# Optimization experiments

Hardware: AMD Instinct MI355X
Metric: run time of the kernel (lower is better)

## Reference

```python
import jax, jax.numpy as jnp
import numpy as np

B=64; HW=14; E=2048; L=30; V=10000; EMB=512; AML=768; ADL=500
D=512+ADL   # decoder_dim + article_downlen = 1012
A=512+ADL   # attention_dim + article_downlen = 1012

def setup_inputs() -> dict:
    key = jax.random.key(0)
    ks = jax.random.split(key, 20)
    s = 0.02
    lin = lambda k, i, o: (jax.random.normal(k, (i, o), jnp.float32) * s)
    inp = {}
    inp['encoder_out'] = jax.random.normal(ks[0], (B, HW, HW, E), jnp.float32)
    inp['encoded_captions'] = jax.random.randint(ks[1], (B, L), 0, V)
    cl = jax.random.randint(ks[2], (B, 1), 2, L + 1)
    inp['caption_lengths'] = cl.at[0, 0].set(L)  # ensure max decode length == L-1
    inp['encoded_articles'] = jax.random.normal(ks[3], (B, 1, AML), jnp.float32)
    inp['article_lengths'] = jax.random.randint(ks[4], (B, 1), 1, AML)
    inp['blank_context'] = 0
    inp['E_emb'] = jax.random.uniform(ks[5], (V, EMB), jnp.float32, -0.1, 0.1)
    inp['W_par'] = lin(ks[6], AML, ADL); inp['b_par'] = jnp.zeros(ADL, jnp.float32)
    inp['W_enc'] = lin(ks[7], E, A);     inp['b_enc'] = jnp.zeros(A, jnp.float32)
    inp['W_dec'] = lin(ks[8], D, A);     inp['b_dec'] = jnp.zeros(A, jnp.float32)
    inp['W_full'] = lin(ks[9], A, 1);    inp['b_full'] = jnp.zeros(1, jnp.float32)
    inp['W_h'] = lin(ks[10], E + ADL, D); inp['b_h'] = jnp.zeros(D, jnp.float32)
    inp['W_c'] = lin(ks[11], E + ADL, D); inp['b_c'] = jnp.zeros(D, jnp.float32)
    inp['W_fb'] = lin(ks[12], D, E);      inp['b_fb'] = jnp.zeros(E, jnp.float32)
    inp['W_ih'] = lin(ks[13], EMB + E, 4 * D); inp['b_ih'] = jnp.zeros(4 * D, jnp.float32)
    inp['W_hh'] = lin(ks[14], D, 4 * D);       inp['b_hh'] = jnp.zeros(4 * D, jnp.float32)
    inp['W_fc'] = jax.random.uniform(ks[15], (D, V), jnp.float32, -0.1, 0.1)
    inp['b_fc'] = jnp.zeros(V, jnp.float32)
    return inp

def reference(encoder_out, encoded_captions, caption_lengths, encoded_articles,
              article_lengths, blank_context, E_emb, W_par, b_par, W_enc, b_enc,
              W_dec, b_dec, W_full, b_full, W_h, b_h, W_c, b_c, W_fb, b_fb,
              W_ih, b_ih, W_hh, b_hh, W_fc, b_fc):
    Bv = encoder_out.shape[0]
    enc = encoder_out.reshape(Bv, -1, encoder_out.shape[-1])  # (B, P, E)
    lens = caption_lengths[:, 0]
    sort_ind = jnp.argsort(-lens)
    lens = lens[sort_ind]
    enc = enc[sort_ind]
    caps = encoded_captions[sort_ind]
    arts = encoded_articles[sort_ind]
    emb = E_emb[caps]                                   # (B, L, EMB)
    context = (arts @ W_par + b_par)[:, 0, :]           # ParagraphEncoder -> (B, ADL)
    dec_in = jnp.concatenate([enc.mean(axis=1), context], axis=1)
    h0 = dec_in @ W_h + b_h
    c0 = dec_in @ W_c + b_c
    dlens = lens - 1
    att1 = enc @ W_enc + b_enc                          # loop-invariant, (B, P, A)
    T = emb.shape[1] - 1

    def step(carry, t):
        h, c = carry
        active = (dlens > t)[:, None]                   # prefix mask (sorted desc)
        att2 = h @ W_dec + b_dec
        scores = (jax.nn.relu(att1 + att2[:, None, :]) @ W_full)[..., 0] + b_full[0]
        alpha = jax.nn.softmax(scores, axis=1)          # (B, P)
        awe = jnp.einsum('bp,bpe->be', alpha, enc)
        awe = jax.nn.sigmoid(h @ W_fb + b_fb) * awe     # gated attention encoding
        x = jnp.concatenate([emb[:, t, :], awe], axis=1)
        gates = x @ W_ih + b_ih + h @ W_hh + b_hh       # torch LSTMCell, gate order i,f,g,o
        i, f, g, o = jnp.split(gates, 4, axis=1)
        c_new = jax.nn.sigmoid(f) * c + jax.nn.sigmoid(i) * jnp.tanh(g)
        h_new = jax.nn.sigmoid(o) * jnp.tanh(c_new)
        preds = jnp.where(active, h_new @ W_fc + b_fc, 0.0)
        alpha_m = jnp.where(active, alpha, 0.0)
        h = jnp.where(active, h_new, h)
        c = jnp.where(active, c_new, c)
        return (h, c), (preds, alpha_m)

    _, (preds, alphas) = jax.lax.scan(step, (h0, c0), jnp.arange(T))
    predictions = jnp.transpose(preds, (1, 0, 2))       # (B, T, V)
    alphas = jnp.transpose(alphas, (1, 0, 2))           # (B, T, P)
    return (predictions, caps, dlens, alphas, sort_ind)
```

## Files before the change

kernel.cpp:

```cpp
#include <hip/hip_runtime.h>
#include <math.h>

#define B_   64
#define P_   196
#define E_   2048
#define L_   30
#define T_   29
#define V_   10000
#define EMB_ 512
#define AML_ 768
#define ADL_ 500
#define D_   1012
#define A_   1012
#define G4_  4048
#define XK_  2560

typedef unsigned short u16;
typedef __attribute__((ext_vector_type(8))) short bf16x8;
typedef __attribute__((ext_vector_type(4))) float f32x4;

__device__ __forceinline__ float sigf(float x) { return 1.f / (1.f + __expf(-x)); }
__device__ __forceinline__ float tanhf_fast(float x) { return 1.f - 2.f / (__expf(2.f * x) + 1.f); }
__device__ __forceinline__ u16 f2bf(float f) {
    unsigned u = __float_as_uint(f);
    return (u16)((u + 0x7FFFu + ((u >> 16) & 1u)) >> 16);
}
__device__ __forceinline__ float bf2f(u16 v) { return __uint_as_float(((unsigned)v) << 16); }

__global__ void k_setup(const int* __restrict__ clen, const int* __restrict__ caps,
                        float* __restrict__ out_caps, float* __restrict__ out_dlens,
                        float* __restrict__ out_sind,
                        int* __restrict__ sort_ind, int* __restrict__ dlens_i,
                        int* __restrict__ nact, int* __restrict__ caps_s)
{
    __shared__ int lens[B_];
    int t = threadIdx.x;
    if (t < B_) lens[t] = clen[t];
    __syncthreads();
    if (t < B_) {
        int my = lens[t];
        int rank = 0;
        for (int j = 0; j < B_; ++j) {
            int lj = lens[j];
            if (lj > my || (lj == my && j < t)) rank++;
        }
        sort_ind[rank] = t;
    }
    __syncthreads();
    if (t < B_) {
        int orig = sort_ind[t];
        int dl = lens[orig] - 1;
        dlens_i[t] = dl;
        out_dlens[t] = (float)dl;
        out_sind[t] = (float)orig;
        for (int j = 0; j < L_; ++j) {
            int cv = caps[orig * L_ + j];
            caps_s[t * L_ + j] = cv;
            out_caps[t * L_ + j] = (float)cv;
        }
    }
    __syncthreads();
    if (t < T_) {
        int cnt = 0;
        for (int j = 0; j < B_; ++j) cnt += (dlens_i[j] > t) ? 1 : 0;
        nact[t] = cnt;
    }
}

__global__ void k_zero(float4* __restrict__ p, long n4)
{
    long i = (long)blockIdx.x * 256 + threadIdx.x;
    if (i < n4) p[i] = make_float4(0.f, 0.f, 0.f, 0.f);
}

__global__ void k_cvt_enc(const float* __restrict__ enc, const int* __restrict__ sort_ind,
                          u16* __restrict__ A_bf)
{
    int row = blockIdx.y;
    int b = row / 196, p = row - b * 196;
    int e4 = (blockIdx.x * 256 + threadIdx.x) * 4;
    const float* src = enc + ((long)sort_ind[b] * 196 + p) * E_ + e4;
    float4 v = *(const float4*)src;
    unsigned lo = (unsigned)f2bf(v.x) | ((unsigned)f2bf(v.y) << 16);
    unsigned hi = (unsigned)f2bf(v.z) | ((unsigned)f2bf(v.w) << 16);
    uint2 pk; pk.x = lo; pk.y = hi;
    *(uint2*)(A_bf + (long)row * E_ + e4) = pk;
}

__global__ void k_transpose(const float* __restrict__ src, u16* __restrict__ dst,
                            int K, int N, int Kp, int Np)
{
    __shared__ float tile[32][33];
    int n0 = blockIdx.x * 32, k0 = blockIdx.y * 32;
    int tx = threadIdx.x, ty = threadIdx.y;
    for (int r = ty; r < 32; r += 8) {
        int k = k0 + r, n = n0 + tx;
        tile[r][tx] = (k < K && n < N) ? src[(long)k * N + n] : 0.f;
    }
    __syncthreads();
    for (int r = ty; r < 32; r += 8) {
        int n = n0 + r, k = k0 + tx;
        if (n < Np && k < Kp) dst[(long)n * Kp + k] = f2bf(tile[tx][r]);
    }
}

__global__ void k_encmean(const float* __restrict__ enc, const int* __restrict__ sort_ind,
                          u16* __restrict__ dec_in)
{
    int b = blockIdx.y;
    int e = blockIdx.x * 256 + threadIdx.x;
    int orig = sort_ind[b];
    const float* src = enc + (long)orig * P_ * E_ + e;
    float s = 0.f;
    for (int p = 0; p < P_; ++p) s += src[(long)p * E_];
    dec_in[(long)b * XK_ + e] = f2bf(s * (1.f / 196.f));
}

__global__ void k_ctx(const float* __restrict__ arts, const float* __restrict__ W_par,
                      const float* __restrict__ b_par, const int* __restrict__ sort_ind,
                      u16* __restrict__ dec_in)
{
    int b = blockIdx.y;
    int k = blockIdx.x * 256 + threadIdx.x;
    if (k >= 512) return;
    float s = 0.f;
    if (k < ADL_) {
        int orig = sort_ind[b];
        const float* ar = arts + (long)orig * AML_;
        s = b_par[k];
        for (int m = 0; m < AML_; ++m) s = fmaf(ar[m], W_par[m * ADL_ + k], s);
    }
    dec_in[(long)b * XK_ + E_ + k] = f2bf(s);
}

__global__ void k_emb_all(const float* __restrict__ E_emb, const int* __restrict__ caps_s,
                          u16* __restrict__ emb_all)
{
    int t = blockIdx.x;
    int b = blockIdx.y;
    int tok = caps_s[b * L_ + t];
    for (int k = threadIdx.x; k < EMB_; k += 256)
        emb_all[((long)t * B_ + b) * EMB_ + k] = f2bf(E_emb[(long)tok * EMB_ + k]);
}

__global__ void __launch_bounds__(256) k_att1_mfma(
    const u16* __restrict__ A, const u16* __restrict__ W,
    const float* __restrict__ bias, u16* __restrict__ Yb)
{
    __shared__ u16 As[2][64][40];
    int w = threadIdx.x >> 6, lane = threadIdx.x & 63;
    int lr = lane & 15, lk = (lane >> 4) * 8;
    int n0 = blockIdx.x * 256 + w * 64;
    int r0 = blockIdx.y * 64;
    int arow = threadIdx.x >> 2;
    int akseg = (threadIdx.x & 3) * 8;
    const u16* ag = A + (long)(r0 + arow) * E_ + akseg;

    f32x4 acc[4][4];
#pragma unroll
    for (int i = 0; i < 4; ++i)
#pragma unroll
        for (int j = 0; j < 4; ++j) acc[i][j] = (f32x4){0.f, 0.f, 0.f, 0.f};
    const u16* wp = W + (long)(n0 + lr) * E_ + lk;

    *(uint2*)&As[0][arow][akseg] = *(const uint2*)(ag);
    __syncthreads();

    for (int k = 0; k < E_; k += 32) {
        int buf = (k >> 5) & 1;
        bool more = (k + 32) < E_;
        uint2 pre;
        if (more) pre = *(const uint2*)(ag + k + 32);
        bf16x8 bf[4], af[4];
#pragma unroll
        for (int nt = 0; nt < 4; ++nt) bf[nt] = *(const bf16x8*)(wp + (long)nt * 16 * E_ + k);
#pragma unroll
        for (int mt = 0; mt < 4; ++mt) af[mt] = *(const bf16x8*)&As[buf][mt * 16 + lr][lk];
#pragma unroll
        for (int mt = 0; mt < 4; ++mt)
#pragma unroll
            for (int nt = 0; nt < 4; ++nt)
                acc[mt][nt] = __builtin_amdgcn_mfma_f32_16x16x32_bf16(af[mt], bf[nt], acc[mt][nt], 0, 0, 0);
        if (more) *(uint2*)&As[buf ^ 1][arow][akseg] = pre;
        __syncthreads();
    }
#pragma unroll
    for (int mt = 0; mt < 4; ++mt) {
#pragma unroll
        for (int nt = 0; nt < 4; ++nt) {
            int n = n0 + nt * 16 + lr;
            float bv = (n < A_) ? bias[n] : 0.f;
#pragma unroll
            for (int j = 0; j < 4; ++j) {
                int row = r0 + mt * 16 + (lane >> 4) * 4 + j;
                u16 outv = (n < A_) ? f2bf(acc[mt][nt][j] + bv) : (u16)0;
                Yb[(long)row * 1024 + n] = outv;
            }
        }
    }
}

template <int ACT, int OUT, int PADZ>
__global__ void __launch_bounds__(256) k_skinny(
    const u16* __restrict__ A1, const u16* __restrict__ W1, int K1,
    const float* __restrict__ bias1, void* __restrict__ Yv,
    long ldY, long offY, int Nmax,
    const int* __restrict__ nact, int t)
{
    int Bact = (t >= 0) ? nact[t] : B_;
    if (Bact <= 0) return;
    int mmax = (Bact + 15) >> 4;
    int w = threadIdx.x >> 6, lane = threadIdx.x & 63;
    int lr = lane & 15, lk = (lane >> 4) * 8;
    int n0 = blockIdx.x * 64 + w * 16;
    f32x4 acc[4];
#pragma unroll
    for (int m = 0; m < 4; ++m) acc[m] = (f32x4){0.f, 0.f, 0.f, 0.f};

    int n = n0 + lr;
    int nc = n < Nmax ? n : Nmax - 1;
    const u16* a1p = A1 + (long)lr * K1 + lk;
    const u16* w1p = W1 + (long)nc * K1 + lk;
    for (int k = 0; k < K1; k += 32) {
        bf16x8 bw = *(const bf16x8*)(w1p + k);
#pragma unroll
        for (int m = 0; m < 4; ++m)
            if (m < mmax) {
                bf16x8 aw = *(const bf16x8*)(a1p + (long)m * 16 * K1 + k);
                acc[m] = __builtin_amdgcn_mfma_f32_16x16x32_bf16(aw, bw, acc[m], 0, 0, 0);
            }
    }
    float bv = (n < Nmax) ? bias1[n] : 0.f;
#pragma unroll
    for (int m = 0; m < 4; ++m) {
        if (m < mmax) {
#pragma unroll
            for (int j = 0; j < 4; ++j) {
                int b = m * 16 + (lane >> 4) * 4 + j;
                if (b < Bact) {
                    float v = acc[m][j] + bv;
                    if (ACT == 1) v = sigf(v);
                    if (n < Nmax) {
                        if (OUT == 1) ((u16*)Yv)[(long)b * ldY + offY + n] = f2bf(v);
                        else          ((float*)Yv)[(long)b * ldY + offY + n] = v;
                    } else if (PADZ) {
                        if (OUT == 1) ((u16*)Yv)[(long)b * ldY + offY + n] = 0;
                        else          ((float*)Yv)[(long)b * ldY + offY + n] = 0.f;
                    }
                }
            }
        }
    }
}

__global__ void __launch_bounds__(256) k_gemb(
    const u16* __restrict__ emb_all, const u16* __restrict__ WT_ih,
    float* __restrict__ gemb_all)
{
    int t = blockIdx.y;
    int w = threadIdx.x >> 6, lane = threadIdx.x & 63;
    int lr = lane & 15, lk = (lane >> 4) * 8;
    int n0 = blockIdx.x * 256 + w * 64;
    f32x4 acc[4][4];
#pragma unroll
    for (int i = 0; i < 4; ++i)
#pragma unroll
        for (int j = 0; j < 4; ++j) acc[i][j] = (f32x4){0.f, 0.f, 0.f, 0.f};
    const u16* ap = emb_all + ((long)t * B_ + lr) * EMB_ + lk;
    long wrow[4];
#pragma unroll
    for (int nt = 0; nt < 4; ++nt) {
        int j = n0 + nt * 16 + lr;
        int q = j >> 10, d = j & 1023;
        wrow[nt] = (long)q * D_ + (d < D_ ? d : D_ - 1);
    }
    for (int k = 0; k < EMB_; k += 32) {
        bf16x8 af[4], bf[4];
#pragma unroll
        for (int mt = 0; mt < 4; ++mt) af[mt] = *(const bf16x8*)(ap + (long)mt * 16 * EMB_ + k);
#pragma unroll
        for (int nt = 0; nt < 4; ++nt) bf[nt] = *(const bf16x8*)(WT_ih + wrow[nt] * XK_ + lk + k);
#pragma unroll
        for (int mt = 0; mt < 4; ++mt)
#pragma unroll
            for (int nt = 0; nt < 4; ++nt)
                acc[mt][nt] = __builtin_amdgcn_mfma_f32_16x16x32_bf16(af[mt], bf[nt], acc[mt][nt], 0, 0, 0);
    }
#pragma unroll
    for (int nt = 0; nt < 4; ++nt) {
        int j = n0 + nt * 16 + lr;
#pragma unroll
        for (int mt = 0; mt < 4; ++mt) {
#pragma unroll
            for (int jj = 0; jj < 4; ++jj) {
                int b = mt * 16 + (lane >> 4) * 4 + jj;
                gemb_all[((long)t * B_ + b) * 4096 + j] = acc[mt][nt][jj];
            }
        }
    }
}

__global__ void __launch_bounds__(256) k_att2fb(
    const u16* __restrict__ h_bf, const u16* __restrict__ WT_dec,
    const u16* __restrict__ WT_fb, const float* __restrict__ b_dec,
    const float* __restrict__ b_fb, float* __restrict__ att2p,
    float* __restrict__ fbp, const int* __restrict__ nact, int t)
{
    int Bact = nact[t];
    if (Bact <= 0) return;
    int mmax = (Bact + 15) >> 4;
    int kh = blockIdx.x >= 48;
    int nb = blockIdx.x - (kh ? 48 : 0);
    int isfb = nb >= 16;
    const u16* W = isfb ? WT_fb : WT_dec;
    const float* bias = isfb ? b_fb : b_dec;
    int Nmax = isfb ? E_ : A_;
    int nb2 = isfb ? nb - 16 : nb;
    long ldY = isfb ? (long)E_ : 1024L;
    float* Y = (isfb ? fbp : att2p) + (long)kh * B_ * ldY;

    int w = threadIdx.x >> 6, lane = threadIdx.x & 63;
    int lr = lane & 15, lk = (lane >> 4) * 8;
    int n = nb2 * 64 + w * 16 + lr;
    int nc = n < Nmax ? n : Nmax - 1;
    int k0 = kh * 512;
    f32x4 acc[4];
#pragma unroll
    for (int m = 0; m < 4; ++m) acc[m] = (f32x4){0.f, 0.f, 0.f, 0.f};
    const u16* ap = h_bf + (long)lr * 1024 + k0 + lk;
    const u16* wp = W + (long)nc * 1024 + k0 + lk;
    for (int k = 0; k < 512; k += 32) {
        bf16x8 bw = *(const bf16x8*)(wp + k);
#pragma unroll
        for (int m = 0; m < 4; ++m)
            if (m < mmax) {
                bf16x8 aw = *(const bf16x8*)(ap + (long)m * 16 * 1024 + k);
                acc[m] = __builtin_amdgcn_mfma_f32_16x16x32_bf16(aw, bw, acc[m], 0, 0, 0);
            }
    }
    if (n >= Nmax) return;
    float bv = (kh == 0) ? bias[n] : 0.f;
#pragma unroll
    for (int m = 0; m < 4; ++m) {
        if (m < mmax) {
#pragma unroll
            for (int j = 0; j < 4; ++j) {
                int b = m * 16 + (lane >> 4) * 4 + j;
                if (b < Bact) Y[(long)b * ldY + n] = acc[m][j] + bv;
            }
        }
    }
}

__global__ void k_scores(const u16* __restrict__ att1, const float* __restrict__ att2p,
                         const float* __restrict__ W_full, const float* __restrict__ b_full,
                         float* __restrict__ scores, const int* __restrict__ nact, int t)
{
    int b = blockIdx.y;
    if (b >= nact[t]) return;
    int wv = threadIdx.x >> 6;
    int lane = threadIdx.x & 63;
    int p = blockIdx.x * 4 + wv;
    const u16* a1 = att1 + ((long)b * P_ + p) * 1024;
    const float* a20 = att2p + (long)b * 1024;
    const float* a21 = att2p + (long)B_ * 1024 + (long)b * 1024;
    float acc = 0.f;
    for (int j2 = lane; j2 < 506; j2 += 64) {
        unsigned pk = *(const unsigned*)(a1 + 2 * j2);
        float2 p0 = *(const float2*)(a20 + 2 * j2);
        float2 p1 = *(const float2*)(a21 + 2 * j2);
        float2 wv2 = *(const float2*)(W_full + 2 * j2);
        float v0 = bf2f((u16)(pk & 0xFFFF)) + p0.x + p1.x;
        float v1 = bf2f((u16)(pk >> 16)) + p0.y + p1.y;
        v0 = v0 > 0.f ? v0 : 0.f;
        v1 = v1 > 0.f ? v1 : 0.f;
        acc = fmaf(v0, wv2.x, acc);
        acc = fmaf(v1, wv2.y, acc);
    }
    for (int m = 32; m >= 1; m >>= 1) acc += __shfl_xor(acc, m);
    if (lane == 0) scores[b * P_ + p] = acc + b_full[0];
}

__global__ void __launch_bounds__(256) k_awe_x(
    const u16* __restrict__ A_bf, const float* __restrict__ scores,
    const float* __restrict__ fbp, u16* __restrict__ awe_buf,
    float* __restrict__ alphas_out, const int* __restrict__ nact, int t)
{
    int b = blockIdx.y;
    if (b >= nact[t]) return;
    int tid = threadIdx.x;
    int w = tid >> 6, lane = tid & 63;
    __shared__ float al[P_];
    __shared__ float red[4];
    float v = (tid < P_) ? scores[b * P_ + tid] : -1e30f;
    float m = v;
    for (int s = 32; s >= 1; s >>= 1) m = fmaxf(m, __shfl_xor(m, s));
    if (lane == 0) red[w] = m;
    __syncthreads();
    m = fmaxf(fmaxf(red[0], red[1]), fmaxf(red[2], red[3]));
    float e = (tid < P_) ? __expf(v - m) : 0.f;
    float s_ = e;
    for (int s = 32; s >= 1; s >>= 1) s_ += __shfl_xor(s_, s);
    __syncthreads();
    if (lane == 0) red[w] = s_;
    __syncthreads();
    s_ = red[0] + red[1] + red[2] + red[3];
    if (tid < P_) al[tid] = e / s_;
    __syncthreads();

    if (blockIdx.x < 8) {
        int e0 = blockIdx.x * 256 + tid;
        const u16* src = A_bf + (long)b * P_ * E_ + e0;
        float s0 = 0.f, s1 = 0.f, s2 = 0.f, s3 = 0.f;
        for (int p = 0; p < P_; p += 4) {
            s0 = fmaf(al[p],     bf2f(src[(long)p * E_]), s0);
            s1 = fmaf(al[p + 1], bf2f(src[(long)(p + 1) * E_]), s1);
            s2 = fmaf(al[p + 2], bf2f(src[(long)(p + 2) * E_]), s2);
            s3 = fmaf(al[p + 3], bf2f(src[(long)(p + 3) * E_]), s3);
        }
        long fb_off = (long)b * E_ + e0;
        float g = sigf(fbp[fb_off] + fbp[131072 + fb_off]);
        awe_buf[(long)b * E_ + e0] = f2bf((s0 + s1 + s2 + s3) * g);
    } else {
        if (tid < P_) alphas_out[((long)b * T_ + t) * P_ + tid] = al[tid];
    }
}

__global__ void __launch_bounds__(256) k_gates(
    const u16* __restrict__ awe, const u16* __restrict__ h_old,
    const u16* __restrict__ WT_ih, const u16* __restrict__ WT_hh,
    float* __restrict__ gpart, const int* __restrict__ nact, int t)
{
    int Bact = nact[t];
    if (Bact <= 0) return;
    int mmax = (Bact + 15) >> 4;
    int q = threadIdx.x >> 6;
    int lane = threadIdx.x & 63;
    int lr = lane & 15, lk = (lane >> 4) * 8;
    int kh = blockIdx.y;
    int n = blockIdx.x * 16 + lr;
    int nc = n < D_ ? n : D_ - 1;
    f32x4 acc[4];
#pragma unroll
    for (int m = 0; m < 4; ++m) acc[m] = (f32x4){0.f, 0.f, 0.f, 0.f};
    const u16* wih = WT_ih + ((long)q * D_ + nc) * XK_;
    const u16* whh = WT_hh + ((long)q * D_ + nc) * 1024;

    if (kh == 0) {
        const u16* ap = awe + (long)lr * E_ + lk;
        const u16* w2 = wih + 512;
        for (int k = 0; k < 1536; k += 32) {
            bf16x8 bw = *(const bf16x8*)(w2 + k);
#pragma unroll
            for (int m = 0; m < 4; ++m)
                if (m < mmax) {
                    bf16x8 aw = *(const bf16x8*)(ap + (long)m * 16 * E_ + k);
                    acc[m] = __builtin_amdgcn_mfma_f32_16x16x32_bf16(aw, bw, acc[m], 0, 0, 0);
                }
        }
    } else {
        const u16* ap2 = awe + (long)lr * E_ + 1536 + lk;
        const u16* w2 = wih + 2048;
        for (int k = 0; k < 512; k += 32) {
            bf16x8 bw = *(const bf16x8*)(w2 + k);
#pragma unroll
            for (int m = 0; m < 4; ++m)
                if (m < mmax) {
                    bf16x8 aw = *(const bf16x8*)(ap2 + (long)m * 16 * E_ + k);
                    acc[m] = __builtin_amdgcn_mfma_f32_16x16x32_bf16(aw, bw, acc[m], 0, 0, 0);
                }
        }
        const u16* ap3 = h_old + (long)lr * 1024 + lk;
        for (int k = 0; k < 1024; k += 32) {
            bf16x8 bw = *(const bf16x8*)(whh + k);
#pragma unroll
            for (int m = 0; m < 4; ++m)
                if (m < mmax) {
                    bf16x8 aw = *(const bf16x8*)(ap3 + (long)m * 16 * 1024 + k);
                    acc[m] = __builtin_amdgcn_mfma_f32_16x16x32_bf16(aw, bw, acc[m], 0, 0, 0);
                }
        }
    }
#pragma unroll
    for (int m = 0; m < 4; ++m) {
        if (m < mmax) {
#pragma unroll
            for (int j = 0; j < 4; ++j) {
                int bb = m * 16 + (lane >> 4) * 4 + j;
                if (bb < Bact)
                    gpart[((long)kh * B_ + bb) * 4096 + q * 1024 + n] = acc[m][j];
            }
        }
    }
}

__global__ void k_lstm_red(const float* __restrict__ gpart, const float* __restrict__ gemb_t,
                           const float* __restrict__ b_ih, const float* __restrict__ b_hh,
                           float* __restrict__ cbuf, u16* __restrict__ h_new,
                           const int* __restrict__ nact, int t)
{
    int b = blockIdx.y;
    if (b >= nact[t]) return;
    int n = blockIdx.x * 256 + threadIdx.x;
    if (n >= D_) return;
    const float* g0 = gpart + (long)b * 4096;
    const float* g1 = gpart + (long)(B_ + b) * 4096;
    const float* ge = gemb_t + (long)b * 4096;
    float gi = g0[n]        + g1[n]        + ge[n]        + b_ih[n]          + b_hh[n];
    float gf = g0[1024 + n] + g1[1024 + n] + ge[1024 + n] + b_ih[D_ + n]     + b_hh[D_ + n];
    float gg = g0[2048 + n] + g1[2048 + n] + ge[2048 + n] + b_ih[2 * D_ + n] + b_hh[2 * D_ + n];
    float go = g0[3072 + n] + g1[3072 + n] + ge[3072 + n] + b_ih[3 * D_ + n] + b_hh[3 * D_ + n];
    float c = cbuf[(long)b * 1024 + n];
    float cn = sigf(gf) * c + sigf(gi) * tanhf_fast(gg);
    float hn = sigf(go) * tanhf_fast(cn);
    cbuf[(long)b * 1024 + n] = cn;
    h_new[(long)b * 1024 + n] = f2bf(hn);
}

__global__ void __launch_bounds__(256) k_fc_all(
    const u16* __restrict__ h_all, const u16* __restrict__ W,
    const float* __restrict__ bias, float* __restrict__ out_preds,
    const int* __restrict__ nact)
{
    int tslot = blockIdx.y;
    int Bact = nact[tslot];
    if (Bact <= 0) return;
    int mmax = (Bact + 15) >> 4;
    int w = threadIdx.x >> 6, lane = threadIdx.x & 63;
    int lr = lane & 15, lk = (lane >> 4) * 8;
    int n0 = blockIdx.x * 256 + w * 64;
    f32x4 acc[4][4];
#pragma unroll
    for (int i = 0; i < 4; ++i)
#pragma unroll
        for (int j = 0; j < 4; ++j) acc[i][j] = (f32x4){0.f, 0.f, 0.f, 0.f};
    const u16* ap = h_all + ((long)(tslot + 1) * B_ + lr) * 1024 + lk;
    int ncl[4];
#pragma unroll
    for (int nt = 0; nt < 4; ++nt) {
        int n = n0 + nt * 16 + lr;
        ncl[nt] = n < V_ ? n : V_ - 1;
    }
    for (int k = 0; k < 1024; k += 32) {
        bf16x8 af[4], bf[4];
#pragma unroll
        for (int mt = 0; mt < 4; ++mt)
            if (mt < mmax) af[mt] = *(const bf16x8*)(ap + (long)mt * 16 * 1024 + k);
#pragma unroll
        for (int nt = 0; nt < 4; ++nt) bf[nt] = *(const bf16x8*)(W + (long)ncl[nt] * 1024 + lk + k);
#pragma unroll
        for (int mt = 0; mt < 4; ++mt)
            if (mt < mmax)
#pragma unroll
                for (int nt = 0; nt < 4; ++nt)
                    acc[mt][nt] = __builtin_amdgcn_mfma_f32_16x16x32_bf16(af[mt], bf[nt], acc[mt][nt], 0, 0, 0);
    }
#pragma unroll
    for (int nt = 0; nt < 4; ++nt) {
        int n = n0 + nt * 16 + lr;
        if (n >= V_) continue;
        float bv = bias[n];
#pragma unroll
        for (int mt = 0; mt < 4; ++mt) {
            if (mt < mmax) {
#pragma unroll
                for (int j = 0; j < 4; ++j) {
                    int b = mt * 16 + (lane >> 4) * 4 + j;
                    if (b < Bact)
                        out_preds[(long)b * T_ * V_ + (long)tslot * V_ + n] = acc[mt][nt][j] + bv;
                }
            }
        }
    }
}

extern "C" void kernel_launch(void* const* d_in, const int* in_sizes, int n_in,
                              void* d_out, int out_size, void* d_ws, size_t ws_size,
                              hipStream_t stream)
{
    const float* enc    = (const float*)d_in[0];
    const int*   caps   = (const int*)d_in[1];
    const int*   clen   = (const int*)d_in[2];
    const float* arts   = (const float*)d_in[3];
    const float* E_emb  = (const float*)d_in[6];
    const float* W_par  = (const float*)d_in[7];
    const float* b_par  = (const float*)d_in[8];
    const float* W_enc  = (const float*)d_in[9];
    const float* b_enc  = (const float*)d_in[10];
    const float* W_dec  = (const float*)d_in[11];
    const float* b_dec  = (const float*)d_in[12];
    const float* W_full = (const float*)d_in[13];
    const float* b_full = (const float*)d_in[14];
    const float* W_h    = (const float*)d_in[15];
    const float* b_h    = (const float*)d_in[16];
    const float* W_c    = (const float*)d_in[17];
    const float* b_c    = (const float*)d_in[18];
    const float* W_fb   = (const float*)d_in[19];
    const float* b_fb   = (const float*)d_in[20];
    const float* W_ih   = (const float*)d_in[21];
    const float* b_ih   = (const float*)d_in[22];
    const float* W_hh   = (const float*)d_in[23];
    const float* b_hh   = (const float*)d_in[24];
    const float* W_fc   = (const float*)d_in[25];
    const float* b_fc   = (const float*)d_in[26];

    float* out = (float*)d_out;
    float* out_preds  = out;
    float* out_caps   = out + (long)B_ * T_ * V_;
    float* out_dlens  = out_caps + B_ * L_;
    float* out_alphas = out_dlens + B_;
    float* out_sind   = out_alphas + (long)B_ * T_ * P_;

    float* ws = (float*)d_ws;
    long o = 0;
    auto alloc = [&](long n) { long r = o; o += (n + 63) & ~63L; return r; };
    long o_ints   = alloc(2176);
    long o_decin  = alloc((long)B_ * XK_ / 2);
    long o_hall   = alloc((long)(T_ + 1) * B_ * 1024 / 2);
    long o_emball = alloc((long)T_ * B_ * EMB_ / 2);
    long o_awe    = alloc((long)B_ * E_ / 2);
    long o_c      = alloc((long)B_ * 1024);
    long o_att2p  = alloc((long)2 * B_ * 1024);
    long o_fbp    = alloc((long)2 * B_ * E_);
    long o_gpart  = alloc((long)2 * B_ * 4096);
    long o_gemb   = alloc((long)T_ * B_ * 4096);
    long o_scores = alloc((long)B_ * P_);
    long o_Abf    = alloc((long)12544 * E_ / 2);
    long o_att1   = alloc((long)12544 * 1024 / 2);
    long o_wtenc  = alloc((long)1024 * 2048 / 2);
    long o_wtdec  = alloc((long)1024 * 1024 / 2);
    long o_wtfb   = alloc((long)2048 * 1024 / 2);
    long o_wtih   = alloc((long)4096 * 2560 / 2);
    long o_wthh   = alloc((long)4096 * 1024 / 2);
    long o_wtfc   = alloc((long)10048 * 1024 / 2);

    int* sort_ind = (int*)(ws + o_ints);
    int* dlens_i  = sort_ind + 64;
    int* nact     = dlens_i + 64;
    int* caps_s   = nact + 32;
    u16*   dec_in  = (u16*)(ws + o_decin);
    u16*   h_all   = (u16*)(ws + o_hall);
    u16*   emb_all = (u16*)(ws + o_emball);
    u16*   awe_buf = (u16*)(ws + o_awe);
    float* cbuf   = ws + o_c;
    float* att2p  = ws + o_att2p;
    float* fbp    = ws + o_fbp;
    float* gpart  = ws + o_gpart;
    float* gemb_all = ws + o_gemb;
    float* scores = ws + o_scores;
    u16*   A_bf   = (u16*)(ws + o_Abf);
    u16*   att1   = (u16*)(ws + o_att1);
    u16*   WT_enc = (u16*)(ws + o_wtenc);
    u16*   WT_dec = (u16*)(ws + o_wtdec);
    u16*   WT_fb  = (u16*)(ws + o_wtfb);
    u16*   WT_ih  = (u16*)(ws + o_wtih);
    u16*   WT_hh  = (u16*)(ws + o_wthh);
    u16*   WT_fc  = (u16*)(ws + o_wtfc);
    u16*   WT_h   = att1;
    u16*   WT_c   = att1 + (long)1024 * XK_;

    long n4 = ((long)B_ * T_ * V_ + B_ * L_ + B_ + (long)B_ * T_ * P_ + B_) / 4;
    k_zero<<<dim3((unsigned)((n4 + 255) / 256)), 256, 0, stream>>>((float4*)d_out, n4);
    k_setup<<<1, 64, 0, stream>>>(clen, caps, out_caps, out_dlens, out_sind,
                                  sort_ind, dlens_i, nact, caps_s);

    k_encmean<<<dim3(8, 64), 256, 0, stream>>>(enc, sort_ind, dec_in);
    k_ctx<<<dim3(2, 64), 256, 0, stream>>>(arts, W_par, b_par, sort_ind, dec_in);
    k_emb_all<<<dim3(T_, 64), 256, 0, stream>>>(E_emb, caps_s, emb_all);

    dim3 tb(32, 8);
    k_transpose<<<dim3(1024/32, 2560/32), tb, 0, stream>>>(W_h, WT_h, 2548, 1012, 2560, 1024);
    k_transpose<<<dim3(1024/32, 2560/32), tb, 0, stream>>>(W_c, WT_c, 2548, 1012, 2560, 1024);
    k_skinny<0,1,1><<<dim3(16), 256, 0, stream>>>(dec_in, WT_h, XK_, b_h, h_all, 1024L, 0L, D_,
                                                  nact, -1);
    k_skinny<0,0,1><<<dim3(16), 256, 0, stream>>>(dec_in, WT_c, XK_, b_c, cbuf, 1024L, 0L, D_,
                                                  nact, -1);

    k_transpose<<<dim3(1024/32, 2048/32), tb, 0, stream>>>(W_enc, WT_enc, 2048, 1012, 2048, 1024);
    k_transpose<<<dim3(1024/32, 1024/32), tb, 0, stream>>>(W_dec, WT_dec, 1012, 1012, 1024, 1024);
    k_transpose<<<dim3(2048/32, 1024/32), tb, 0, stream>>>(W_fb, WT_fb, 1012, 2048, 1024, 2048);
    k_transpose<<<dim3(4096/32, 2560/32), tb, 0, stream>>>(W_ih, WT_ih, 2560, 4048, 2560, 4096);
    k_transpose<<<dim3(4096/32, 1024/32), tb, 0, stream>>>(W_hh, WT_hh, 1012, 4048, 1024, 4096);
    k_transpose<<<dim3(10048/32, 1024/32), tb, 0, stream>>>(W_fc, WT_fc, 1012, 10000, 1024, 10048);

    k_cvt_enc<<<dim3(2, 12544), 256, 0, stream>>>(enc, sort_ind, A_bf);
    k_att1_mfma<<<dim3(4, 196), 256, 0, stream>>>(A_bf, WT_enc, b_enc, att1);
    k_gemb<<<dim3(16, T_), 256, 0, stream>>>(emb_all, WT_ih, gemb_all);

    for (int t = 0; t < T_; ++t) {
        const u16* h_old = h_all + (long)t * B_ * 1024;
        u16* h_new = h_all + (long)(t + 1) * B_ * 1024;
        const float* gemb_t = gemb_all + (long)t * B_ * 4096;
        k_att2fb<<<dim3(96), 256, 0, stream>>>(h_old, WT_dec, WT_fb, b_dec, b_fb,
                                               att2p, fbp, nact, t);
        k_scores<<<dim3(49, 64), 256, 0, stream>>>(att1, att2p, W_full, b_full, scores, nact, t);
        k_awe_x<<<dim3(9, 64), 256, 0, stream>>>(A_bf, scores, fbp, awe_buf,
                                                 out_alphas, nact, t);
        k_gates<<<dim3(64, 2), 256, 0, stream>>>(awe_buf, h_old, WT_ih, WT_hh, gpart, nact, t);
        k_lstm_red<<<dim3(4, 64), 256, 0, stream>>>(gpart, gemb_t, b_ih, b_hh, cbuf, h_new,
                                                    nact, t);
    }
    k_fc_all<<<dim3(40, T_), 256, 0, stream>>>(h_all, WT_fc, b_fc, out_preds, nact);
}
```

Baseline: 2.847 ms.

## Move h·W_hh into att2/fb kernel and fuse LSTM reduction into gates

The recurrent h@W_hh product is now computed in the kernel that already reads h for att2 and the gate signal, as 128 extra blocks that write partial sums to a new ghp buffer. This leaves the gates kernel with a balanced 1024+1024 split over the awe part of W_ih. The separate LSTM elementwise kernel is removed: the last of the two k-split blocks per column tile, found with an atomic counter, sums all partials and applies the cell update. The goal is one fewer launch per step and better balanced work on the critical path, at the cost of a threadfence/atomic handshake and an extra partial buffer. The att1 GEMM tile load is also widened from uint2 to uint4, so each thread now fills its full 8-element slice of the shared tile.

Measured after the change: 2.979 ms. 4.6% more time.

```diff
diff --git a/kernel.cpp b/kernel.cpp
--- a/kernel.cpp
+++ b/kernel.cpp
@@ -31,11 +31,13 @@
                         float* __restrict__ out_caps, float* __restrict__ out_dlens,
                         float* __restrict__ out_sind,
                         int* __restrict__ sort_ind, int* __restrict__ dlens_i,
-                        int* __restrict__ nact, int* __restrict__ caps_s)
+                        int* __restrict__ nact, int* __restrict__ caps_s,
+                        int* __restrict__ gcnt)
 {
     __shared__ int lens[B_];
     int t = threadIdx.x;
     if (t < B_) lens[t] = clen[t];
+    if (t < 64) gcnt[t] = 0;
     __syncthreads();
     if (t < B_) {
         int my = lens[t];
@@ -163,14 +165,14 @@
         for (int j = 0; j < 4; ++j) acc[i][j] = (f32x4){0.f, 0.f, 0.f, 0.f};
     const u16* wp = W + (long)(n0 + lr) * E_ + lk;
 
-    *(uint2*)&As[0][arow][akseg] = *(const uint2*)(ag);
+    *(uint4*)&As[0][arow][akseg] = *(const uint4*)(ag);
     __syncthreads();
 
     for (int k = 0; k < E_; k += 32) {
         int buf = (k >> 5) & 1;
         bool more = (k + 32) < E_;
-        uint2 pre;
-        if (more) pre = *(const uint2*)(ag + k + 32);
+        uint4 pre;
+        if (more) pre = *(const uint4*)(ag + k + 32);
         bf16x8 bf[4], af[4];
 #pragma unroll
         for (int nt = 0; nt < 4; ++nt) bf[nt] = *(const bf16x8*)(wp + (long)nt * 16 * E_ + k);
@@ -181,7 +183,7 @@
 #pragma unroll
             for (int nt = 0; nt < 4; ++nt)
                 acc[mt][nt] = __builtin_amdgcn_mfma_f32_16x16x32_bf16(af[mt], bf[nt], acc[mt][nt], 0, 0, 0);
-        if (more) *(uint2*)&As[buf ^ 1][arow][akseg] = pre;
+        if (more) *(uint4*)&As[buf ^ 1][arow][akseg] = pre;
         __syncthreads();
     }
 #pragma unroll
@@ -300,53 +302,89 @@
     }
 }
 
-__global__ void __launch_bounds__(256) k_att2fb(
+__global__ void __launch_bounds__(256) k_hg(
     const u16* __restrict__ h_bf, const u16* __restrict__ WT_dec,
-    const u16* __restrict__ WT_fb, const float* __restrict__ b_dec,
-    const float* __restrict__ b_fb, float* __restrict__ att2p,
-    float* __restrict__ fbp, const int* __restrict__ nact, int t)
+    const u16* __restrict__ WT_fb, const u16* __restrict__ WT_hh,
+    const float* __restrict__ b_dec, const float* __restrict__ b_fb,
+    float* __restrict__ att2p, float* __restrict__ fbp, float* __restrict__ ghp,
+    const int* __restrict__ nact, int t)
 {
     int Bact = nact[t];
     if (Bact <= 0) return;
     int mmax = (Bact + 15) >> 4;
-    int kh = blockIdx.x >= 48;
-    int nb = blockIdx.x - (kh ? 48 : 0);
-    int isfb = nb >= 16;
-    const u16* W = isfb ? WT_fb : WT_dec;
-    const float* bias = isfb ? b_fb : b_dec;
-    int Nmax = isfb ? E_ : A_;
-    int nb2 = isfb ? nb - 16 : nb;
-    long ldY = isfb ? (long)E_ : 1024L;
-    float* Y = (isfb ? fbp : att2p) + (long)kh * B_ * ldY;
-
     int w = threadIdx.x >> 6, lane = threadIdx.x & 63;
     int lr = lane & 15, lk = (lane >> 4) * 8;
-    int n = nb2 * 64 + w * 16 + lr;
-    int nc = n < Nmax ? n : Nmax - 1;
-    int k0 = kh * 512;
-    f32x4 acc[4];
-#pragma unroll
-    for (int m = 0; m < 4; ++m) acc[m] = (f32x4){0.f, 0.f, 0.f, 0.f};
-    const u16* ap = h_bf + (long)lr * 1024 + k0 + lk;
-    const u16* wp = W + (long)nc * 1024 + k0 + lk;
-    for (int k = 0; k < 512; k += 32) {
-        bf16x8 bw = *(const bf16x8*)(wp + k);
-#pragma unroll
-        for (int m = 0; m < 4; ++m)
+
+    if (blockIdx.x < 96) {
+        int kh = blockIdx.x >= 48;
+        int nb = blockIdx.x - (kh ? 48 : 0);
+        int isfb = nb >= 16;
+        const u16* W = isfb ? WT_fb : WT_dec;
+        const float* bias = isfb ? b_fb : b_dec;
+        int Nmax = isfb ? E_ : A_;
+        int nb2 = isfb ? nb - 16 : nb;
+        long ldY = isfb ? (long)E_ : 1024L;
+        float* Y = (isfb ? fbp : att2p) + (long)kh * B_ * ldY;
+
+        int n = nb2 * 64 + w * 16 + lr;
+        int nc = n < Nmax ? n : Nmax - 1;
+        int k0 = kh * 512;
+        f32x4 acc[4];
+#pragma unroll
+        for (int m = 0; m < 4; ++m) acc[m] = (f32x4){0.f, 0.f, 0.f, 0.f};
+        const u16* ap = h_bf + (long)lr * 1024 + k0 + lk;
+        const u16* wp = W + (long)nc * 1024 + k0 + lk;
+        for (int k = 0; k < 512; k += 32) {
+            bf16x8 bw = *(const bf16x8*)(wp + k);
+#pragma unroll
+            for (int m = 0; m < 4; ++m)
+                if (m < mmax) {
+                    bf16x8 aw = *(const bf16x8*)(ap + (long)m * 16 * 1024 + k);
+                    acc[m] = __builtin_amdgcn_mfma_f32_16x16x32_bf16(aw, bw, acc[m], 0, 0, 0);
+                }
+        }
+        if (n >= Nmax) return;
+        float bv = (kh == 0) ? bias[n] : 0.f;
+#pragma unroll
+        for (int m = 0; m < 4; ++m) {
             if (m < mmax) {
-                bf16x8 aw = *(const bf16x8*)(ap + (long)m * 16 * 1024 + k);
-                acc[m] = __builtin_amdgcn_mfma_f32_16x16x32_bf16(aw, bw, acc[m], 0, 0, 0);
-            }
-    }
-    if (n >= Nmax) return;
-    float bv = (kh == 0) ? bias[n] : 0.f;
-#pragma unroll
-    for (int m = 0; m < 4; ++m) {
-        if (m < mmax) {
-#pragma unroll
-            for (int j = 0; j < 4; ++j) {
-                int b = m * 16 + (lane >> 4) * 4 + j;
-                if (b < Bact) Y[(long)b * ldY + n] = acc[m][j] + bv;
+#pragma unroll
+                for (int j = 0; j < 4; ++j) {
+                    int b = m * 16 + (lane >> 4) * 4 + j;
+                    if (b < Bact) Y[(long)b * ldY + n] = acc[m][j] + bv;
+                }
+            }
+        }
+    } else {
+        int u = blockIdx.x - 96;
+        int kh2 = u >> 6, nb = u & 63;
+        int q = w;
+        int n = nb * 16 + lr;
+        int nc = n < D_ ? n : D_ - 1;
+        int k0 = kh2 * 512;
+        f32x4 acc[4];
+#pragma unroll
+        for (int m = 0; m < 4; ++m) acc[m] = (f32x4){0.f, 0.f, 0.f, 0.f};
+        const u16* ap = h_bf + (long)lr * 1024 + k0 + lk;
+        const u16* wp = WT_hh + ((long)q * D_ + nc) * 1024 + k0 + lk;
+        for (int k = 0; k < 512; k += 32) {
+            bf16x8 bw = *(const bf16x8*)(wp + k);
+#pragma unroll
+            for (int m = 0; m < 4; ++m)
+                if (m < mmax) {
+                    bf16x8 aw = *(const bf16x8*)(ap + (long)m * 16 * 1024 + k);
+                    acc[m] = __builtin_amdgcn_mfma_f32_16x16x32_bf16(aw, bw, acc[m], 0, 0, 0);
+                }
+        }
+#pragma unroll
+        for (int m = 0; m < 4; ++m) {
+            if (m < mmax) {
+#pragma unroll
+                for (int j = 0; j < 4; ++j) {
+                    int bb = m * 16 + (lane >> 4) * 4 + j;
+                    if (bb < Bact)
+                        ghp[((long)kh2 * B_ + bb) * 4096 + q * 1024 + n] = acc[m][j];
+                }
             }
         }
     }
@@ -426,10 +464,13 @@
     }
 }
 
-__global__ void __launch_bounds__(256) k_gates(
-    const u16* __restrict__ awe, const u16* __restrict__ h_old,
-    const u16* __restrict__ WT_ih, const u16* __restrict__ WT_hh,
-    float* __restrict__ gpart, const int* __restrict__ nact, int t)
+__global__ void __launch_bounds__(256) k_gates_lstm(
+    const u16* __restrict__ awe, const u16* __restrict__ WT_ih,
+    const float* __restrict__ ghp, const float* __restrict__ gemb_t,
+    const float* __restrict__ b_ih, const float* __restrict__ b_hh,
+    float* __restrict__ gpart, int* __restrict__ gcnt,
+    float* __restrict__ cbuf, u16* __restrict__ h_new,
+    const int* __restrict__ nact, int t)
 {
     int Bact = nact[t];
     if (Bact <= 0) return;
@@ -437,49 +478,22 @@
     int q = threadIdx.x >> 6;
     int lane = threadIdx.x & 63;
     int lr = lane & 15, lk = (lane >> 4) * 8;
-    int kh = blockIdx.y;
-    int n = blockIdx.x * 16 + lr;
+    int nblk = blockIdx.x, kh = blockIdx.y;
+    int n = nblk * 16 + lr;
     int nc = n < D_ ? n : D_ - 1;
     f32x4 acc[4];
 #pragma unroll
     for (int m = 0; m < 4; ++m) acc[m] = (f32x4){0.f, 0.f, 0.f, 0.f};
-    const u16* wih = WT_ih + ((long)q * D_ + nc) * XK_;
-    const u16* whh = WT_hh + ((long)q * D_ + nc) * 1024;
-
-    if (kh == 0) {
-        const u16* ap = awe + (long)lr * E_ + lk;
-        const u16* w2 = wih + 512;
-        for (int k = 0; k < 1536; k += 32) {
-            bf16x8 bw = *(const bf16x8*)(w2 + k);
-#pragma unroll
-            for (int m = 0; m < 4; ++m)
-                if (m < mmax) {
-                    bf16x8 aw = *(const bf16x8*)(ap + (long)m * 16 * E_ + k);
-                    acc[m] = __builtin_amdgcn_mfma_f32_16x16x32_bf16(aw, bw, acc[m], 0, 0, 0);
-                }
-        }
-    } else {
-        const u16* ap2 = awe + (long)lr * E_ + 1536 + lk;
-        const u16* w2 = wih + 2048;
-        for (int k = 0; k < 512; k += 32) {
-            bf16x8 bw = *(const bf16x8*)(w2 + k);
-#pragma unroll
-            for (int m = 0; m < 4; ++m)
-                if (m < mmax) {
-                    bf16x8 aw = *(const bf16x8*)(ap2 + (long)m * 16 * E_ + k);
-                    acc[m] = __builtin_amdgcn_mfma_f32_16x16x32_bf16(aw, bw, acc[m], 0, 0, 0);
-                }
-        }
-        const u16* ap3 = h_old + (long)lr * 1024 + lk;
-        for (int k = 0; k < 1024; k += 32) {
-            bf16x8 bw = *(const bf16x8*)(whh + k);
-#pragma unroll
-            for (int m = 0; m < 4; ++m)
-                if (m < mmax) {
-                    bf16x8 aw = *(const bf16x8*)(ap3 + (long)m * 16 * 1024 + k);
-                    acc[m] = __builtin_amdgcn_mfma_f32_16x16x32_bf16(aw, bw, acc[m], 0, 0, 0);
-                }
-        }
+    const u16* wp = WT_ih + ((long)q * D_ + nc) * XK_ + 512 + kh * 1024;
+    const u16* ap = awe + (long)lr * E_ + kh * 1024 + lk;
+    for (int k = 0; k < 1024; k += 32) {
+        bf16x8 bw = *(const bf16x8*)(wp + k);
+#pragma unroll
+        for (int m = 0; m < 4; ++m)
+            if (m < mmax) {
+                bf16x8 aw = *(const bf16x8*)(ap + (long)m * 16 * E_ + k);
+                acc[m] = __builtin_amdgcn_mfma_f32_16x16x32_bf16(aw, bw, acc[m], 0, 0, 0);
+            }
     }
 #pragma unroll
     for (int m = 0; m < 4; ++m) {
@@ -492,29 +506,40 @@
             }
         }
     }
-}
-
-__global__ void k_lstm_red(const float* __restrict__ gpart, const float* __restrict__ gemb_t,
-                           const float* __restrict__ b_ih, const float* __restrict__ b_hh,
-                           float* __restrict__ cbuf, u16* __restrict__ h_new,
-                           const int* __restrict__ nact, int t)
-{
-    int b = blockIdx.y;
-    if (b >= nact[t]) return;
-    int n = blockIdx.x * 256 + threadIdx.x;
-    if (n >= D_) return;
-    const float* g0 = gpart + (long)b * 4096;
-    const float* g1 = gpart + (long)(B_ + b) * 4096;
-    const float* ge = gemb_t + (long)b * 4096;
-    float gi = g0[n]        + g1[n]        + ge[n]        + b_ih[n]          + b_hh[n];
-    float gf = g0[1024 + n] + g1[1024 + n] + ge[1024 + n] + b_ih[D_ + n]     + b_hh[D_ + n];
-    float gg = g0[2048 + n] + g1[2048 + n] + ge[2048 + n] + b_ih[2 * D_ + n] + b_hh[2 * D_ + n];
-    float go = g0[3072 + n] + g1[3072 + n] + ge[3072 + n] + b_ih[3 * D_ + n] + b_hh[3 * D_ + n];
-    float c = cbuf[(long)b * 1024 + n];
-    float cn = sigf(gf) * c + sigf(gi) * tanhf_fast(gg);
-    float hn = sigf(go) * tanhf_fast(cn);
-    cbuf[(long)b * 1024 + n] = cn;
-    h_new[(long)b * 1024 + n] = f2bf(hn);
+    __threadfence();
+    __syncthreads();
+    __shared__ int isLast;
+    if (threadIdx.x == 0) isLast = (atomicAdd(&gcnt[nblk], 1) == 1) ? 1 : 0;
+    __syncthreads();
+    if (!isLast) return;
+    __threadfence();
+#pragma unroll
+    for (int i = 0; i < 4; ++i) {
+        int idx = threadIdx.x + i * 256;
+        int bb = idx >> 4, col = idx & 15;
+        if (bb >= Bact) continue;
+        int n2 = nblk * 16 + col;
+        if (n2 >= D_) continue;
+        const float* gp0 = gpart + (long)bb * 4096 + n2;
+        const float* gp1 = gpart + (long)(B_ + bb) * 4096 + n2;
+        const float* gh0 = ghp + (long)bb * 4096 + n2;
+        const float* gh1 = ghp + (long)(B_ + bb) * 4096 + n2;
+        const float* ge  = gemb_t + (long)bb * 4096 + n2;
+        float gi = gp0[0]    + gp1[0]    + gh0[0]    + gh1[0]    + ge[0]
+                 + b_ih[n2]          + b_hh[n2];
+        float gf = gp0[1024] + gp1[1024] + gh0[1024] + gh1[1024] + ge[1024]
+                 + b_ih[D_ + n2]     + b_hh[D_ + n2];
+        float gg = gp0[2048] + gp1[2048] + gh0[2048] + gh1[2048] + ge[2048]
+                 + b_ih[2 * D_ + n2] + b_hh[2 * D_ + n2];
+        float go = gp0[3072] + gp1[3072] + gh0[3072] + gh1[3072] + ge[3072]
+                 + b_ih[3 * D_ + n2] + b_hh[3 * D_ + n2];
+        float c = cbuf[(long)bb * 1024 + n2];
+        float cn = sigf(gf) * c + sigf(gi) * tanhf_fast(gg);
+        float hn = sigf(go) * tanhf_fast(cn);
+        cbuf[(long)bb * 1024 + n2] = cn;
+        h_new[(long)bb * 1024 + n2] = f2bf(hn);
+    }
+    if (threadIdx.x == 0) atomicExch(&gcnt[nblk], 0);
 }
 
 __global__ void __launch_bounds__(256) k_fc_all(
@@ -614,7 +639,7 @@
     float* ws = (float*)d_ws;
     long o = 0;
     auto alloc = [&](long n) { long r = o; o += (n + 63) & ~63L; return r; };
-    long o_ints   = alloc(2176);
+    long o_ints   = alloc(2240);
     long o_decin  = alloc((long)B_ * XK_ / 2);
     long o_hall   = alloc((long)(T_ + 1) * B_ * 1024 / 2);
     long o_emball = alloc((long)T_ * B_ * EMB_ / 2);
@@ -622,6 +647,7 @@
     long o_c      = alloc((long)B_ * 1024);
     long o_att2p  = alloc((long)2 * B_ * 1024);
     long o_fbp    = alloc((long)2 * B_ * E_);
+    long o_ghp    = alloc((long)2 * B_ * 4096);
     long o_gpart  = alloc((long)2 * B_ * 4096);
     long o_gemb   = alloc((long)T_ * B_ * 4096);
     long o_scores = alloc((long)B_ * P_);
@@ -638,6 +664,7 @@
     int* dlens_i  = sort_ind + 64;
     int* nact     = dlens_i + 64;
     int* caps_s   = nact + 32;
+    int* gcnt     = caps_s + B_ * L_;
     u16*   dec_in  = (u16*)(ws + o_decin);
     u16*   h_all   = (u16*)(ws + o_hall);
     u16*   emb_all = (u16*)(ws + o_emball);
@@ -645,6 +672,7 @@
     float* cbuf   = ws + o_c;
     float* att2p  = ws + o_att2p;
     float* fbp    = ws + o_fbp;
+    float* ghp    = ws + o_ghp;
     float* gpart  = ws + o_gpart;
     float* gemb_all = ws + o_gemb;
     float* scores = ws + o_scores;
@@ -662,7 +690,7 @@
     long n4 = ((long)B_ * T_ * V_ + B_ * L_ + B_ + (long)B_ * T_ * P_ + B_) / 4;
     k_zero<<<dim3((unsigned)((n4 + 255) / 256)), 256, 0, stream>>>((float4*)d_out, n4);
     k_setup<<<1, 64, 0, stream>>>(clen, caps, out_caps, out_dlens, out_sind,
-                                  sort_ind, dlens_i, nact, caps_s);
+                                  sort_ind, dlens_i, nact, caps_s, gcnt);
 
     k_encmean<<<dim3(8, 64), 256, 0, stream>>>(enc, sort_ind, dec_in);
     k_ctx<<<dim3(2, 64), 256, 0, stream>>>(arts, W_par, b_par, sort_ind, dec_in);
@@ -691,14 +719,14 @@
         const u16* h_old = h_all + (long)t * B_ * 1024;
         u16* h_new = h_all + (long)(t + 1) * B_ * 1024;
         const float* gemb_t = gemb_all + (long)t * B_ * 4096;
-        k_att2fb<<<dim3(96), 256, 0, stream>>>(h_old, WT_dec, WT_fb, b_dec, b_fb,
-                                               att2p, fbp, nact, t);
+        k_hg<<<dim3(224), 256, 0, stream>>>(h_old, WT_dec, WT_fb, WT_hh, b_dec, b_fb,
+                                            att2p, fbp, ghp, nact, t);
         k_scores<<<dim3(49, 64), 256, 0, stream>>>(att1, att2p, W_full, b_full, scores, nact, t);
         k_awe_x<<<dim3(9, 64), 256, 0, stream>>>(A_bf, scores, fbp, awe_buf,
                                                  out_alphas, nact, t);
-        k_gates<<<dim3(64, 2), 256, 0, stream>>>(awe_buf, h_old, WT_ih, WT_hh, gpart, nact, t);
-        k_lstm_red<<<dim3(4, 64), 256, 0, stream>>>(gpart, gemb_t, b_ih, b_hh, cbuf, h_new,
-                                                    nact, t);
+        k_gates_lstm<<<dim3(64, 2), 256, 0, stream>>>(awe_buf, WT_ih, ghp, gemb_t,
+                                                      b_ih, b_hh, gpart, gcnt, cbuf, h_new,
+                                                      nact, t);
     }
     k_fc_all<<<dim3(40, T_), 256, 0, stream>>>(h_all, WT_fc, b_fc, out_preds, nact);
 }
```
